# Kernel optimization log

Hardware: AMD Instinct MI355X
Metric: run time of the kernel (lower is better)

The kernel has to match this reference:

```python
import jax, jax.numpy as jnp
import numpy as np

B, S, E, H = 4, 512, 512, 8
DH = E // H
HID = max(16, E // 4)  # sr_ratio=4
ALPHA = 0.1
EPS_SAFE = 0.05  # eps=1e-6 clamped to [0.05, 0.8]


def _xavier(k, shape):
    fan_out, fan_in = shape[0], shape[1]
    lim = (6.0 / (fan_in + fan_out)) ** 0.5
    return jax.random.uniform(k, shape, minval=-lim, maxval=lim, dtype=jnp.float32)


def setup_inputs() -> dict:
    key = jax.random.key(0)
    ks = jax.random.split(key, 8)
    return {
        "x": jax.random.normal(ks[0], (B, S, E), dtype=jnp.float32),
        "wq": _xavier(ks[1], (E, E)), "bq": jnp.zeros((E,), jnp.float32),
        "wk": _xavier(ks[2], (E, E)), "bk": jnp.zeros((E,), jnp.float32),
        "wv": _xavier(ks[3], (E, E)), "bv": jnp.zeros((E,), jnp.float32),
        "wo": _xavier(ks[4], (E, E)), "bo": jnp.zeros((E,), jnp.float32),
        # sr_conv1: Conv2d(1, HID, 1) -> weight [HID,1,1,1] == vector [HID]
        "w1": _xavier(ks[5], (HID, 1)).reshape(HID), "b1": jnp.zeros((HID,), jnp.float32),
        # sr_conv2: Conv2d(HID, 1, 1) -> weight [1,HID,1,1] == vector [HID]
        "w2": _xavier(ks[6], (1, HID)).reshape(HID), "b2": jnp.zeros((), jnp.float32),
    }


def _autopoietic_transform(scores, w1, b1, w2, b2):
    # scores: [B, H, S, S]
    scores = jnp.clip(jnp.nan_to_num(scores, nan=0.0, posinf=10.0, neginf=-10.0), -15.0, 15.0)
    mean_attn = scores.mean(axis=1)  # mean over heads -> [B, S, S]

    scaled = jnp.clip(jnp.clip(mean_attn, -8.0, 8.0) * EPS_SAFE, -10.0, 10.0)
    # conv1x1 (1 -> HID): broadcastmul; clamp + relu; conv1x1 (HID -> 1)
    hid = scaled[:, None, :, :] * w1[None, :, None, None] + b1[None, :, None, None]  # [B,HID,S,S]
    hid = jax.nn.relu(jnp.clip(hid, -5.0, 5.0))
    auto = jnp.einsum('bhij,h->bij', hid, w2) + b2  # [B,S,S]
    auto = jnp.clip(auto, -5.0, 5.0)

    # Taylor expansion with clamp, then sigmoid smoothing
    taylor = jnp.clip(1.0 + 0.05 * (auto * 50.0), 0.5, 1.5)
    sig = jax.nn.sigmoid(taylor)

    # fuzzy probability via entropy of softmax of mean attention
    p = jax.nn.softmax(jnp.clip(mean_attn, -10.0, 10.0), axis=-1)
    Hent = -p * jnp.log(p + 1e-6)
    Fm = jax.nn.softmax(3.0 * Hent, axis=-1)

    t = sig * Fm

    # energy (Frobenius-norm) balancing per batch
    e_o = jnp.sqrt((mean_attn ** 2).sum(axis=(1, 2))) + 1e-4
    e_t = jnp.sqrt((t ** 2).sum(axis=(1, 2))) + 1e-4
    gamma = jnp.clip(e_o / e_t, 0.8, 1.2)[:, None, None]
    t = gamma * t

    # dynamic std matching
    t_mean = t.mean(axis=(1, 2), keepdims=True)
    o_mean = mean_attn.mean(axis=(1, 2), keepdims=True)
    t_std = jnp.sqrt(jnp.clip(((t - t_mean) ** 2).mean(axis=(1, 2), keepdims=True), 0.01, None))
    o_std = jnp.sqrt(jnp.clip(((mean_attn - o_mean) ** 2).mean(axis=(1, 2), keepdims=True), 0.01, None))
    gdyn = jnp.clip(o_std / t_std, 0.8, 1.2)
    t = o_mean + gdyn * (t - t_mean)

    # residual blend of transformed map back into per-head scores (alpha=0.1), final clamp
    return jnp.clip(scores + ALPHA * t[:, None, :, :], -15.0, 15.0)


def reference(x, wq, bq, wk, bk, wv, bv, wo, bo, w1, b1, w2, b2):
    scaling = DH ** -0.5
    q = (jnp.einsum('bse,oe->bso', x, wq) + bq).reshape(B, S, H, DH).transpose(0, 2, 1, 3) * scaling
    k = (jnp.einsum('bse,oe->bso', x, wk) + bk).reshape(B, S, H, DH).transpose(0, 2, 1, 3)
    v = (jnp.einsum('bse,oe->bso', x, wv) + bv).reshape(B, S, H, DH).transpose(0, 2, 1, 3)
    scores = jnp.einsum('bhqd,bhkd->bhqk', q, k)  # [B,H,S,S]
    scores = _autopoietic_transform(scores, w1, b1, w2, b2)
    attn = jax.nn.softmax(scores, axis=-1)
    out = jnp.einsum('bhqk,bhkd->bhqd', attn, v).transpose(0, 2, 1, 3).reshape(B, S, E)
    return jnp.einsum('bse,oe->bso', out, wo) + bo
```

## Files before the change

kernel.cpp:

```cpp
#include <hip/hip_runtime.h>
#include <math.h>

#define BATCH 4
#define SEQ   512
#define EMB   512
#define NH    8
#define DHD   64
#define HIDN  128
#define ALPHA 0.1f
#define EPSS  0.05f

#define LUTN  2048
#define XMIN  (-0.4f)
#define XSTEP (0.8f / LUTN)

typedef __attribute__((ext_vector_type(8))) short  bf16x8;
typedef __attribute__((ext_vector_type(4))) float  f32x4;
#define MFMA(a,b,c) __builtin_amdgcn_mfma_f32_16x16x32_bf16((a),(b),(c),0,0,0)

__device__ __forceinline__ unsigned short f2bf(float f) {
    union { float f; unsigned u; } v; v.f = f;
    unsigned r = v.u + 0x7fffu + ((v.u >> 16) & 1u);
    return (unsigned short)(r >> 16);
}
__device__ __forceinline__ float bf2f(unsigned short h) {
    union { unsigned u; float f; } v; v.u = ((unsigned)h) << 16;
    return v.f;
}
__device__ __forceinline__ float f16tof(unsigned short h) {
    union { unsigned short s; _Float16 f; } v; v.s = h; return (float)v.f;
}
__device__ __forceinline__ unsigned short ftof16(float f) {
    union { unsigned short s; _Float16 f; } v; v.f = (_Float16)f; return v.s;
}

__device__ __forceinline__ void async_lds16(const unsigned short* g, unsigned short* l) {
    __builtin_amdgcn_global_load_lds(
        (const __attribute__((address_space(1))) void*)g,
        (__attribute__((address_space(3))) void*)l, 16, 0, 0);
}

template<int KS, int UN, int MT>
__device__ __forceinline__ void gemm_core64(
    const unsigned short* __restrict__ A, const unsigned short* __restrict__ B,
    int m0, int n0, unsigned short* sA, unsigned short* sB, f32x4 (&acc)[2][4])
{
    const int K = KS * 64;
    const int tid = threadIdx.x, w = tid >> 6, lane = tid & 63;
    const int quad = lane >> 4, r = lane & 15;
    const int wm = w >> 1, wn = w & 1;
    const int lrow = lane >> 3, lc = lane & 7;
    const int sc = lc ^ lrow;
    constexpr int AF = MT / 32;
    constexpr int NB = UN;

    const unsigned short* ag[2]; unsigned short* dAu[2];
    #pragma unroll
    for (int c = 0; c < AF; c++) {
        const int rb = w * (8 * AF) + c * 8;
        ag[c]  = A + (long)(m0 + rb + lrow) * K + sc * 8;
        dAu[c] = sA + rb * 64;
    }
    const unsigned short* bg[4]; unsigned short* dBu[4];
    #pragma unroll
    for (int c = 0; c < NB; c++) {
        const int rb = w * (8 * NB) + c * 8;
        bg[c]  = B + (long)(n0 + rb + lrow) * K + sc * 8;
        dBu[c] = sB + rb * 64;
    }

    for (int s = 0; s < KS; s++) {
        const int k0 = s * 64;
        #pragma unroll
        for (int c = 0; c < AF; c++) async_lds16(ag[c] + k0, dAu[c]);
        #pragma unroll
        for (int c = 0; c < NB; c++) async_lds16(bg[c] + k0, dBu[c]);
        __syncthreads();
        #pragma unroll
        for (int kc = 0; kc < 2; kc++) {
            bf16x8 af[2], bfr[4];
            #pragma unroll
            for (int t = 0; t < AF; t++) {
                const int row = wm * (16 * AF) + t * 16 + r;
                af[t] = *(const bf16x8*)(sA + row * 64 + ((kc * 4 + quad) ^ (row & 7)) * 8);
            }
            #pragma unroll
            for (int u = 0; u < UN; u++) {
                const int row = wn * (16 * UN) + u * 16 + r;
                bfr[u] = *(const bf16x8*)(sB + row * 64 + ((kc * 4 + quad) ^ (row & 7)) * 8);
            }
            #pragma unroll
            for (int t = 0; t < AF; t++)
                #pragma unroll
                for (int u = 0; u < UN; u++)
                    acc[t][u] = MFMA(af[t], bfr[u], acc[t][u]);
        }
        __syncthreads();
    }
}

__global__ __launch_bounds__(256) void gemm_qkv(
    const unsigned short* __restrict__ x_ext, const unsigned short* __restrict__ w_ext,
    const float* __restrict__ bq, const float* __restrict__ bk, const float* __restrict__ bv,
    unsigned short* __restrict__ q_ext, unsigned short* __restrict__ k_ext,
    unsigned short* __restrict__ vT)
{
    __shared__ __align__(16) unsigned char smem[64 * 68 * 4];
    unsigned short* sA = (unsigned short*)smem;
    unsigned short* sB = (unsigned short*)(smem + 64 * 64 * 2);
    float* sC = (float*)smem;

    const int m0 = blockIdx.y * 64, n0 = blockIdx.x * 64;
    f32x4 acc[2][4] = {};
    gemm_core64<24, 2, 64>(x_ext, w_ext, m0, n0, sA, sB, acc);

    const int tid = threadIdx.x, w = tid >> 6, lane = tid & 63;
    const int quad = lane >> 4, r = lane & 15;
    const int wm = w >> 1, wn = w & 1;
    #pragma unroll
    for (int t = 0; t < 2; t++)
        #pragma unroll
        for (int u = 0; u < 2; u++)
            #pragma unroll
            for (int g = 0; g < 4; g++)
                sC[(wm * 32 + t * 16 + quad * 4 + g) * 68 + wn * 32 + u * 16 + r] = acc[t][u][g];
    __syncthreads();

    const int which = n0 >> 9;
    const int n0l = n0 & 511;
    const int h0 = n0l >> 6;
    const int b = m0 >> 9, s0 = m0 & 511;

    if (which < 2) {
        const float scl = (which == 0) ? 0.125f : 1.0f;
        const float* bias = (which == 0) ? bq : bk;
        unsigned* dst = (unsigned*)((which == 0) ? q_ext : k_ext);
        #pragma unroll
        for (int seg = 0; seg < 3; seg++) {
            const bool lo = (which == 0) ? (seg == 1) : (seg == 2);
            #pragma unroll
            for (int it = 0; it < 8; it++) {
                const int idx = it * 256 + tid;
                const int sl = idx >> 5;
                const int jc = idx & 31;
                const int nc = jc * 2;
                float v0 = (sC[sl * 68 + nc]     + bias[n0l + nc])     * scl;
                float v1 = (sC[sl * 68 + nc + 1] + bias[n0l + nc + 1]) * scl;
                unsigned short a0 = f2bf(v0), a1 = f2bf(v1);
                if (lo) { a0 = f2bf(v0 - bf2f(a0)); a1 = f2bf(v1 - bf2f(a1)); }
                const long orow = (long)(b * NH + h0) * SEQ + s0 + sl;
                dst[orow * 96 + seg * 32 + jc] = (unsigned)a0 | ((unsigned)a1 << 16);
            }
        }
    } else {
        unsigned* dst = (unsigned*)vT;
        #pragma unroll
        for (int it = 0; it < 8; it++) {
            const int idx = it * 256 + tid;
            const int d = idx >> 5;
            const int jc = idx & 31;
            const int sl = jc * 2;
            const float bvv = bv[n0l + d];
            const float v0 = sC[sl * 68 + d] + bvv;
            const float v1 = sC[(sl + 1) * 68 + d] + bvv;
            const long orow = (long)(b * NH + h0) * DHD + d;
            dst[orow * 256 + (s0 >> 1) + jc] = (unsigned)f2bf(v0) | ((unsigned)f2bf(v1) << 16);
        }
    }
}

__global__ __launch_bounds__(256) void gemm_scores(
    const unsigned short* __restrict__ q_ext, const unsigned short* __restrict__ k_ext,
    unsigned short* __restrict__ scoresH)
{
    __shared__ __align__(16) unsigned short sA[64 * 64];
    __shared__ __align__(16) unsigned short sB[128 * 64];
    const int z = blockIdx.z;
    const int m0 = blockIdx.y * 64, n0 = blockIdx.x * 128;
    f32x4 acc[2][4] = {};
    gemm_core64<3, 4, 64>(q_ext + (long)z * SEQ * 192, k_ext + (long)z * SEQ * 192,
                          m0, n0, sA, sB, acc);

    const int tid = threadIdx.x, w = tid >> 6, lane = tid & 63;
    const int quad = lane >> 4, r = lane & 15;
    const int wm = w >> 1, wn = w & 1;
    unsigned short* hC = sB;
    #pragma unroll
    for (int t = 0; t < 2; t++)
        #pragma unroll
        for (int u = 0; u < 4; u++)
            #pragma unroll
            for (int g = 0; g < 4; g++) {
                const int ml = wm * 32 + t * 16 + quad * 4 + g;
                const int nl = wn * 64 + u * 16 + r;
                hC[ml * 128 + nl] = ftof16(fminf(fmaxf(acc[t][u][g], -15.f), 15.f));
            }
    __syncthreads();
    #pragma unroll
    for (int it = 0; it < 4; it++) {
        const int id = it * 256 + tid;
        const int ml = id >> 4, ch = id & 15;
        *(uint4*)(scoresH + ((long)z * SEQ + m0 + ml) * SEQ + n0 + ch * 8) =
            *(const uint4*)(hC + ml * 128 + ch * 8);
    }
}

__global__ __launch_bounds__(256) void gemm_proj(
    const unsigned short* __restrict__ otmp, const unsigned short* __restrict__ woh,
    const float* __restrict__ bo, float* __restrict__ out)
{
    __shared__ __align__(16) unsigned short sA[32 * 64];
    __shared__ __align__(16) unsigned short sB[64 * 64];
    const int m0 = blockIdx.y * 32, n0 = blockIdx.x * 64;
    f32x4 acc[2][4] = {};
    gemm_core64<8, 2, 32>(otmp, woh, m0, n0, sA, sB, acc);
    const int tid = threadIdx.x, w = tid >> 6, lane = tid & 63;
    const int quad = lane >> 4, r = lane & 15;
    const int wm = w >> 1, wn = w & 1;
    #pragma unroll
    for (int u = 0; u < 2; u++)
        #pragma unroll
        for (int g = 0; g < 4; g++) {
            const int m = m0 + wm * 16 + quad * 4 + g;
            const int n = n0 + wn * 32 + u * 16 + r;
            out[(long)m * EMB + n] = acc[0][u][g] + bo[n];
        }
}

__device__ __forceinline__ float blockReduceSum(float v, float* sred) {
    #pragma unroll
    for (int o = 32; o > 0; o >>= 1) v += __shfl_down(v, o);
    __syncthreads();
    if ((threadIdx.x & 63) == 0) sred[threadIdx.x >> 6] = v;
    __syncthreads();
    return (sred[0] + sred[1]) + (sred[2] + sred[3]);
}
__device__ __forceinline__ float4 blockReduceSum4(float4 v, float4* s4) {
    #pragma unroll
    for (int o = 32; o > 0; o >>= 1) {
        v.x += __shfl_down(v.x, o); v.y += __shfl_down(v.y, o);
        v.z += __shfl_down(v.z, o); v.w += __shfl_down(v.w, o);
    }
    __syncthreads();
    if ((threadIdx.x & 63) == 0) s4[threadIdx.x >> 6] = v;
    __syncthreads();
    float4 r;
    r.x = (s4[0].x + s4[1].x) + (s4[2].x + s4[3].x);
    r.y = (s4[0].y + s4[1].y) + (s4[2].y + s4[3].y);
    r.z = (s4[0].z + s4[1].z) + (s4[2].z + s4[3].z);
    r.w = (s4[0].w + s4[1].w) + (s4[2].w + s4[3].w);
    return r;
}

__global__ __launch_bounds__(256) void prep_kernel(
    const float* __restrict__ x,
    const float* __restrict__ wq, const float* __restrict__ wk,
    const float* __restrict__ wv, const float* __restrict__ wo,
    const float* __restrict__ w1, const float* __restrict__ b1,
    const float* __restrict__ w2, const float* __restrict__ b2,
    unsigned short* __restrict__ x_ext, unsigned short* __restrict__ w_ext,
    unsigned short* __restrict__ woh, float* __restrict__ lut)
{
    const int blk = blockIdx.x;
    if (blk < 9) {
        const int i = blk * 256 + threadIdx.x;
        if (i > LUTN) return;
        const float xv = XMIN + i * XSTEP;
        float a = 0.f;
        for (int h = 0; h < HIDN; h++) {
            float hv = xv * w1[h] + b1[h];
            hv = fminf(fmaxf(hv, -5.f), 5.f);
            hv = fmaxf(hv, 0.f);
            a += hv * w2[h];
        }
        a += b2[0];
        a = fminf(fmaxf(a, -5.f), 5.f);
        const float taylor = fminf(fmaxf(1.f + 2.5f * a, 0.5f), 1.5f);
        lut[i] = 1.f / (1.f + expf(-taylor));
        return;
    }
    const int i = (blk - 9) * 256 + threadIdx.x;
    if (i < 262144) {
        const int m = i >> 7, kq = i & 127;
        const float4 v = ((const float4*)x)[i];
        const unsigned short h0 = f2bf(v.x), h1 = f2bf(v.y), h2 = f2bf(v.z), h3 = f2bf(v.w);
        const unsigned hi01 = (unsigned)h0 | ((unsigned)h1 << 16);
        const unsigned hi23 = (unsigned)h2 | ((unsigned)h3 << 16);
        const unsigned lo01 = (unsigned)f2bf(v.x - bf2f(h0)) | ((unsigned)f2bf(v.y - bf2f(h1)) << 16);
        const unsigned lo23 = (unsigned)f2bf(v.z - bf2f(h2)) | ((unsigned)f2bf(v.w - bf2f(h3)) << 16);
        unsigned* dst = (unsigned*)x_ext;
        const long base = (long)m * 768 + kq * 2;
        dst[base] = hi01;       dst[base + 1] = hi23;
        dst[base + 256] = lo01; dst[base + 257] = lo23;
        dst[base + 512] = hi01; dst[base + 513] = hi23;
    } else if (i < 458752) {
        const int j = i - 262144;
        const int n = j >> 7, kq = j & 127;
        const float4 v = (j < 65536) ? ((const float4*)wq)[j]
                       : (j < 131072 ? ((const float4*)wk)[j - 65536]
                                     : ((const float4*)wv)[j - 131072]);
        const unsigned short h0 = f2bf(v.x), h1 = f2bf(v.y), h2 = f2bf(v.z), h3 = f2bf(v.w);
        const unsigned hi01 = (unsigned)h0 | ((unsigned)h1 << 16);
        const unsigned hi23 = (unsigned)h2 | ((unsigned)h3 << 16);
        const unsigned lo01 = (unsigned)f2bf(v.x - bf2f(h0)) | ((unsigned)f2bf(v.y - bf2f(h1)) << 16);
        const unsigned lo23 = (unsigned)f2bf(v.z - bf2f(h2)) | ((unsigned)f2bf(v.w - bf2f(h3)) << 16);
        unsigned* dst = (unsigned*)w_ext;
        const long base = (long)n * 768 + kq * 2;
        dst[base] = hi01;       dst[base + 1] = hi23;
        dst[base + 256] = hi01; dst[base + 257] = hi23;
        dst[base + 512] = lo01; dst[base + 513] = lo23;
    } else {
        const int j = i - 458752;
        const float4 v = ((const float4*)wo)[j];
        unsigned* dst = (unsigned*)woh;
        dst[j * 2]     = (unsigned)f2bf(v.x) | ((unsigned)f2bf(v.y) << 16);
        dst[j * 2 + 1] = (unsigned)f2bf(v.z) | ((unsigned)f2bf(v.w) << 16);
    }
}

__global__ __launch_bounds__(256) void transform_kernel(
    const unsigned short* __restrict__ scoresH,
    const float* __restrict__ lut,
    unsigned short* __restrict__ t0H,
    float4* __restrict__ partials)
{
    const int rr = blockIdx.x;
    const int b = rr >> 9, i = rr & 511;
    const int tid = threadIdx.x;

    __shared__ float slut[LUTN + 1];
    __shared__ float sred[4];
    __shared__ float4 sred4[4];

    for (int u = tid; u <= LUTN; u += 256) slut[u] = lut[u];

    const unsigned* baseU =
        (const unsigned*)(scoresH + (((long)(b * NH)) * SEQ + i) * SEQ) + tid;
    float s0 = 0.f, s1 = 0.f;
    #pragma unroll
    for (int h = 0; h < NH; h++) {
        const unsigned pv = baseU[h * (SEQ * SEQ / 2)];
        s0 += f16tof((unsigned short)pv);
        s1 += f16tof((unsigned short)(pv >> 16));
    }
    float mv[2] = { s0 * 0.125f, s1 * 0.125f };
    __syncthreads();

    float sigv[2], ex[2];
    float lsum = 0.f;
    #pragma unroll
    for (int u = 0; u < 2; u++) {
        const float m = mv[u];
        const float x = fminf(fmaxf(m, -8.f), 8.f) * EPSS;
        float t = (x - XMIN) * (1.0f / XSTEP);
        int idx = (int)t;
        idx = idx < 0 ? 0 : (idx > LUTN - 1 ? LUTN - 1 : idx);
        const float frac = t - (float)idx;
        const float l0 = slut[idx], l1 = slut[idx + 1];
        sigv[u] = l0 + frac * (l1 - l0);
        ex[u] = expf(fminf(fmaxf(m, -10.f), 10.f));
        lsum += ex[u];
    }
    const float rsum = blockReduceSum(lsum, sred);
    const float inv = 1.f / rsum;

    float ex2[2], lsum2 = 0.f;
    #pragma unroll
    for (int u = 0; u < 2; u++) {
        const float p = ex[u] * inv;
        const float he = -p * logf(p + 1e-6f);
        ex2[u] = expf(3.f * he);
        lsum2 += ex2[u];
    }
    const float rsum2 = blockReduceSum(lsum2, sred);
    const float inv2 = 1.f / rsum2;

    float tv[2];
    #pragma unroll
    for (int u = 0; u < 2; u++) tv[u] = sigv[u] * (ex2[u] * inv2);
    ((unsigned*)t0H)[((long)b * SEQ + i) * (SEQ / 2) + tid] =
        (unsigned)ftof16(tv[0]) | ((unsigned)ftof16(tv[1]) << 16);

    float4 pv;
    pv.x = mv[0] + mv[1];
    pv.y = mv[0] * mv[0] + mv[1] * mv[1];
    pv.z = tv[0] + tv[1];
    pv.w = tv[0] * tv[0] + tv[1] * tv[1];
    const float4 rs = blockReduceSum4(pv, sred4);
    if (tid == 0) partials[rr] = rs;
}

__global__ __launch_bounds__(256) void softmax_attnv(
    const unsigned short* __restrict__ scoresH,
    const unsigned short* __restrict__ t0H,
    const float4* __restrict__ partials,
    const unsigned short* __restrict__ vT,
    unsigned short* __restrict__ otmp)
{
    __shared__ __align__(16) unsigned char smem[40960];
    unsigned short* attnS = (unsigned short*)smem;
    unsigned short* sB    = (unsigned short*)(smem + 32768);
    float*  sC    = (float*)smem;
    float4* sred4 = (float4*)smem;

    const int m0 = blockIdx.x * 32;
    const int z  = blockIdx.y;
    const int b  = z >> 3, h = z & 7;
    const int tid = threadIdx.x, wv = tid >> 6, lane = tid & 63;

    const float4 p0 = partials[b * SEQ + tid];
    const float4 p1 = partials[b * SEQ + tid + 256];
    float4 pv4 = make_float4(p0.x + p1.x, p0.y + p1.y, p0.z + p1.z, p0.w + p1.w);
    const float4 rs4 = blockReduceSum4(pv4, sred4);
    const float sm = rs4.x, sm2 = rs4.y, st = rs4.z, st2 = rs4.w;
    const float n = (float)SEQ * (float)SEQ;
    const float gamma = fminf(fmaxf((sqrtf(sm2) + 1e-4f) / (sqrtf(st2) + 1e-4f), 0.8f), 1.2f);
    const float o_mean = sm / n, t0m = st / n;
    const float o_std = sqrtf(fmaxf(fmaxf(sm2 / n - o_mean * o_mean, 0.f), 0.01f));
    const float t_std = sqrtf(fmaxf(gamma * gamma * fmaxf(st2 / n - t0m * t0m, 0.f), 0.01f));
    const float gdyn = fminf(fmaxf(o_std / t_std, 0.8f), 1.2f);
    const float c1 = gdyn * gamma;
    const float c0 = o_mean - c1 * t0m;
    __syncthreads();

    const int lrow = lane >> 3, lc = lane & 7;
    const int scw = lc ^ lrow;
    const unsigned short* bg0 = vT + (long)z * DHD * SEQ + (long)(wv * 16 + lrow) * SEQ + scw * 8;
    const unsigned short* bg1 = bg0 + 8 * SEQ;
    unsigned short* dB0 = sB + (wv * 16) * 64;
    unsigned short* dB1 = sB + (wv * 16 + 8) * 64;
    async_lds16(bg0, dB0);
    async_lds16(bg1, dB1);

    const int j0 = lane * 8;
    for (int it = 0; it < 8; it++) {
        const int rowl = it * 4 + wv;
        const bf16x8 sr = *(const bf16x8*)(scoresH + ((long)z * SEQ + m0 + rowl) * SEQ + j0);
        const bf16x8 tr = *(const bf16x8*)(t0H + ((long)b * SEQ + m0 + rowl) * SEQ + j0);
        float sv[8];
        float lsum = 0.f;
        #pragma unroll
        for (int u = 0; u < 8; u++) {
            float s = f16tof((unsigned short)sr[u])
                    + ALPHA * (c0 + c1 * f16tof((unsigned short)tr[u]));
            s = fminf(fmaxf(s, -15.f), 15.f);
            sv[u] = expf(s);
            lsum += sv[u];
        }
        #pragma unroll
        for (int o = 32; o > 0; o >>= 1) lsum += __shfl_down(lsum, o);
        lsum = __shfl(lsum, 0);
        const float inv = 1.f / lsum;
        bf16x8 pk;
        #pragma unroll
        for (int u = 0; u < 8; u++) pk[u] = (short)f2bf(sv[u] * inv);
        *(bf16x8*)(attnS + rowl * 512 + (j0 ^ ((rowl & 7) << 3))) = pk;
    }

    const int quad = lane >> 4, r = lane & 15;
    const int wm = wv >> 1, wn = wv & 1;
    const int arow = wm * 16 + r;
    const int aswz = (arow & 7) << 3;
    f32x4 acc[2] = {};
    for (int s = 0; s < 8; s++) {
        __syncthreads();
        const int k0 = s * 64;
        #pragma unroll
        for (int kc = 0; kc < 2; kc++) {
            const bf16x8 a = *(const bf16x8*)(attnS + arow * 512 + ((k0 + kc * 32 + quad * 8) ^ aswz));
            #pragma unroll
            for (int u = 0; u < 2; u++) {
                const int row = wn * 32 + u * 16 + r;
                const bf16x8 bb = *(const bf16x8*)(sB + row * 64 + ((kc * 4 + quad) ^ (row & 7)) * 8);
                acc[u] = MFMA(a, bb, acc[u]);
            }
        }
        __syncthreads();
        if (s < 7) { async_lds16(bg0 + (s + 1) * 64, dB0); async_lds16(bg1 + (s + 1) * 64, dB1); }
    }

    #pragma unroll
    for (int u = 0; u < 2; u++)
        #pragma unroll
        for (int g = 0; g < 4; g++)
            sC[(wm * 16 + quad * 4 + g) * 66 + wn * 32 + u * 16 + r] = acc[u][g];
    __syncthreads();
    unsigned* dst = (unsigned*)otmp;
    #pragma unroll
    for (int it = 0; it < 4; it++) {
        const int idx = it * 256 + tid;
        const int sr2 = idx >> 5, jc = idx & 31;
        const float v0 = sC[sr2 * 66 + jc * 2], v1 = sC[sr2 * 66 + jc * 2 + 1];
        dst[((long)(b * SEQ + m0 + sr2)) * 256 + h * 32 + jc] =
            (unsigned)f2bf(v0) | ((unsigned)f2bf(v1) << 16);
    }
}

extern "C" void kernel_launch(void* const* d_in, const int* in_sizes, int n_in,
                              void* d_out, int out_size, void* d_ws, size_t ws_size,
                              hipStream_t stream) {
    const float* x  = (const float*)d_in[0];
    const float* wq = (const float*)d_in[1];
    const float* bq = (const float*)d_in[2];
    const float* wk = (const float*)d_in[3];
    const float* bk = (const float*)d_in[4];
    const float* wv = (const float*)d_in[5];
    const float* bv = (const float*)d_in[6];
    const float* wo = (const float*)d_in[7];
    const float* bo = (const float*)d_in[8];
    const float* w1 = (const float*)d_in[9];
    const float* b1 = (const float*)d_in[10];
    const float* w2 = (const float*)d_in[11];
    const float* b2 = (const float*)d_in[12];
    float* out = (float*)d_out;

    char* wsb = (char*)d_ws;
    unsigned short* scoresH = (unsigned short*)wsb;
    unsigned short* t0H     = scoresH + 8388608;
    float4* partials = (float4*)(t0H + 1048576);
    float*  lutbuf   = (float*)(partials + 2048);
    unsigned short* u16 = (unsigned short*)(wsb + (20u << 20));
    unsigned short* x_ext = u16;
    unsigned short* w_ext = x_ext + 3145728;
    unsigned short* q_ext = w_ext + 2359296;
    unsigned short* k_ext = q_ext + 3145728;
    unsigned short* vT    = k_ext + 3145728;
    unsigned short* otmp  = vT + 1048576;
    unsigned short* woh   = otmp + 1048576;

    prep_kernel<<<dim3(9 + 2048), dim3(256), 0, stream>>>(
        x, wq, wk, wv, wo, w1, b1, w2, b2, x_ext, w_ext, woh, lutbuf);

    gemm_qkv<<<dim3(24, 32), dim3(256), 0, stream>>>(
        x_ext, w_ext, bq, bk, bv, q_ext, k_ext, vT);

    gemm_scores<<<dim3(4, 8, 32), dim3(256), 0, stream>>>(q_ext, k_ext, scoresH);

    transform_kernel<<<dim3(BATCH * SEQ), dim3(256), 0, stream>>>(
        scoresH, lutbuf, t0H, partials);

    softmax_attnv<<<dim3(16, 32), dim3(256), 0, stream>>>(
        scoresH, t0H, partials, vT, otmp);

    gemm_proj<<<dim3(8, 64), dim3(256), 0, stream>>>(otmp, woh, bo, out);
}
```

Before: 145.5 us.

## Fuse output projection into attention kernel via per-head atomic accumulation

The separate output-projection GEMM is removed. Each attention block now multiplies its 32x64 per-head output tile by the matching 64-column slice of Wo and atomically adds the result into the zero-initialised output, with the bias added only by head 0. The transform kernel is also changed to handle four rows per block so the LUT is loaded into shared memory fewer times. This drops one launch and the otmp round-trip through memory, but adds a memset, eight-way float atomic contention per output element, uncached Wo reads straight from global memory, and nondeterministic summation order.

```diff
diff --git a/kernel.cpp b/kernel.cpp
--- a/kernel.cpp
+++ b/kernel.cpp
@@ -203,28 +203,6 @@
         *(uint4*)(scoresH + ((long)z * SEQ + m0 + ml) * SEQ + n0 + ch * 8) =
             *(const uint4*)(hC + ml * 128 + ch * 8);
     }
-}
-
-__global__ __launch_bounds__(256) void gemm_proj(
-    const unsigned short* __restrict__ otmp, const unsigned short* __restrict__ woh,
-    const float* __restrict__ bo, float* __restrict__ out)
-{
-    __shared__ __align__(16) unsigned short sA[32 * 64];
-    __shared__ __align__(16) unsigned short sB[64 * 64];
-    const int m0 = blockIdx.y * 32, n0 = blockIdx.x * 64;
-    f32x4 acc[2][4] = {};
-    gemm_core64<8, 2, 32>(otmp, woh, m0, n0, sA, sB, acc);
-    const int tid = threadIdx.x, w = tid >> 6, lane = tid & 63;
-    const int quad = lane >> 4, r = lane & 15;
-    const int wm = w >> 1, wn = w & 1;
-    #pragma unroll
-    for (int u = 0; u < 2; u++)
-        #pragma unroll
-        for (int g = 0; g < 4; g++) {
-            const int m = m0 + wm * 16 + quad * 4 + g;
-            const int n = n0 + wn * 32 + u * 16 + r;
-            out[(long)m * EMB + n] = acc[0][u][g] + bo[n];
-        }
 }
 
 __device__ __forceinline__ float blockReduceSum(float v, float* sred) {
@@ -324,8 +302,6 @@
     unsigned short* __restrict__ t0H,
     float4* __restrict__ partials)
 {
-    const int rr = blockIdx.x;
-    const int b = rr >> 9, i = rr & 511;
     const int tid = threadIdx.x;
 
     __shared__ float slut[LUTN + 1];
@@ -333,74 +309,81 @@
     __shared__ float4 sred4[4];
 
     for (int u = tid; u <= LUTN; u += 256) slut[u] = lut[u];
-
-    const unsigned* baseU =
-        (const unsigned*)(scoresH + (((long)(b * NH)) * SEQ + i) * SEQ) + tid;
-    float s0 = 0.f, s1 = 0.f;
-    #pragma unroll
-    for (int h = 0; h < NH; h++) {
-        const unsigned pv = baseU[h * (SEQ * SEQ / 2)];
-        s0 += f16tof((unsigned short)pv);
-        s1 += f16tof((unsigned short)(pv >> 16));
-    }
-    float mv[2] = { s0 * 0.125f, s1 * 0.125f };
-    __syncthreads();
-
-    float sigv[2], ex[2];
-    float lsum = 0.f;
-    #pragma unroll
-    for (int u = 0; u < 2; u++) {
-        const float m = mv[u];
-        const float x = fminf(fmaxf(m, -8.f), 8.f) * EPSS;
-        float t = (x - XMIN) * (1.0f / XSTEP);
-        int idx = (int)t;
-        idx = idx < 0 ? 0 : (idx > LUTN - 1 ? LUTN - 1 : idx);
-        const float frac = t - (float)idx;
-        const float l0 = slut[idx], l1 = slut[idx + 1];
-        sigv[u] = l0 + frac * (l1 - l0);
-        ex[u] = expf(fminf(fmaxf(m, -10.f), 10.f));
-        lsum += ex[u];
-    }
-    const float rsum = blockReduceSum(lsum, sred);
-    const float inv = 1.f / rsum;
-
-    float ex2[2], lsum2 = 0.f;
-    #pragma unroll
-    for (int u = 0; u < 2; u++) {
-        const float p = ex[u] * inv;
-        const float he = -p * logf(p + 1e-6f);
-        ex2[u] = expf(3.f * he);
-        lsum2 += ex2[u];
-    }
-    const float rsum2 = blockReduceSum(lsum2, sred);
-    const float inv2 = 1.f / rsum2;
-
-    float tv[2];
-    #pragma unroll
-    for (int u = 0; u < 2; u++) tv[u] = sigv[u] * (ex2[u] * inv2);
-    ((unsigned*)t0H)[((long)b * SEQ + i) * (SEQ / 2) + tid] =
-        (unsigned)ftof16(tv[0]) | ((unsigned)ftof16(tv[1]) << 16);
-
-    float4 pv;
-    pv.x = mv[0] + mv[1];
-    pv.y = mv[0] * mv[0] + mv[1] * mv[1];
-    pv.z = tv[0] + tv[1];
-    pv.w = tv[0] * tv[0] + tv[1] * tv[1];
-    const float4 rs = blockReduceSum4(pv, sred4);
-    if (tid == 0) partials[rr] = rs;
-}
-
-__global__ __launch_bounds__(256) void softmax_attnv(
+    __syncthreads();
+
+    for (int r4 = 0; r4 < 4; r4++) {
+        const int rr = blockIdx.x * 4 + r4;
+        const int b = rr >> 9, i = rr & 511;
+
+        const unsigned* baseU =
+            (const unsigned*)(scoresH + (((long)(b * NH)) * SEQ + i) * SEQ) + tid;
+        float s0 = 0.f, s1 = 0.f;
+        #pragma unroll
+        for (int h = 0; h < NH; h++) {
+            const unsigned pv = baseU[h * (SEQ * SEQ / 2)];
+            s0 += f16tof((unsigned short)pv);
+            s1 += f16tof((unsigned short)(pv >> 16));
+        }
+        float mv[2] = { s0 * 0.125f, s1 * 0.125f };
+
+        float sigv[2], ex[2];
+        float lsum = 0.f;
+        #pragma unroll
+        for (int u = 0; u < 2; u++) {
+            const float m = mv[u];
+            const float x = fminf(fmaxf(m, -8.f), 8.f) * EPSS;
+            float t = (x - XMIN) * (1.0f / XSTEP);
+            int idx = (int)t;
+            idx = idx < 0 ? 0 : (idx > LUTN - 1 ? LUTN - 1 : idx);
+            const float frac = t - (float)idx;
+            const float l0 = slut[idx], l1 = slut[idx + 1];
+            sigv[u] = l0 + frac * (l1 - l0);
+            ex[u] = expf(fminf(fmaxf(m, -10.f), 10.f));
+            lsum += ex[u];
+        }
+        const float rsum = blockReduceSum(lsum, sred);
+        const float inv = 1.f / rsum;
+
+        float ex2[2], lsum2 = 0.f;
+        #pragma unroll
+        for (int u = 0; u < 2; u++) {
+            const float p = ex[u] * inv;
+            const float he = -p * logf(p + 1e-6f);
+            ex2[u] = expf(3.f * he);
+            lsum2 += ex2[u];
+        }
+        const float rsum2 = blockReduceSum(lsum2, sred);
+        const float inv2 = 1.f / rsum2;
+
+        float tv[2];
+        #pragma unroll
+        for (int u = 0; u < 2; u++) tv[u] = sigv[u] * (ex2[u] * inv2);
+        ((unsigned*)t0H)[((long)b * SEQ + i) * (SEQ / 2) + tid] =
+            (unsigned)ftof16(tv[0]) | ((unsigned)ftof16(tv[1]) << 16);
+
+        float4 pv;
+        pv.x = mv[0] + mv[1];
+        pv.y = mv[0] * mv[0] + mv[1] * mv[1];
+        pv.z = tv[0] + tv[1];
+        pv.w = tv[0] * tv[0] + tv[1] * tv[1];
+        const float4 rs = blockReduceSum4(pv, sred4);
+        if (tid == 0) partials[rr] = rs;
+    }
+}
+
+__global__ __launch_bounds__(256) void softmax_attnv_proj(
     const unsigned short* __restrict__ scoresH,
     const unsigned short* __restrict__ t0H,
     const float4* __restrict__ partials,
     const unsigned short* __restrict__ vT,
-    unsigned short* __restrict__ otmp)
+    const unsigned short* __restrict__ woh,
+    const float* __restrict__ bo,
+    float* __restrict__ out)
 {
     __shared__ __align__(16) unsigned char smem[40960];
     unsigned short* attnS = (unsigned short*)smem;
     unsigned short* sB    = (unsigned short*)(smem + 32768);
-    float*  sC    = (float*)smem;
+    unsigned short* oA    = (unsigned short*)smem;
     float4* sred4 = (float4*)smem;
 
     const int m0 = blockIdx.x * 32;
@@ -483,16 +466,31 @@
     for (int u = 0; u < 2; u++)
         #pragma unroll
         for (int g = 0; g < 4; g++)
-            sC[(wm * 16 + quad * 4 + g) * 66 + wn * 32 + u * 16 + r] = acc[u][g];
-    __syncthreads();
-    unsigned* dst = (unsigned*)otmp;
-    #pragma unroll
-    for (int it = 0; it < 4; it++) {
-        const int idx = it * 256 + tid;
-        const int sr2 = idx >> 5, jc = idx & 31;
-        const float v0 = sC[sr2 * 66 + jc * 2], v1 = sC[sr2 * 66 + jc * 2 + 1];
-        dst[((long)(b * SEQ + m0 + sr2)) * 256 + h * 32 + jc] =
-            (unsigned)f2bf(v0) | ((unsigned)f2bf(v1) << 16);
+            oA[(wm * 16 + quad * 4 + g) * 72 + wn * 32 + u * 16 + r] = f2bf(acc[u][g]);
+    __syncthreads();
+
+    for (int nc = 0; nc < 8; nc++) {
+        f32x4 acc2[2] = {};
+        #pragma unroll
+        for (int kc = 0; kc < 2; kc++) {
+            const bf16x8 a = *(const bf16x8*)(oA + (wm * 16 + r) * 72 + kc * 32 + quad * 8);
+            #pragma unroll
+            for (int u = 0; u < 2; u++) {
+                const int nrow = nc * 64 + wn * 32 + u * 16 + r;
+                const bf16x8 bb = *(const bf16x8*)(woh + (long)nrow * EMB + h * 64 + kc * 32 + quad * 8);
+                acc2[u] = MFMA(a, bb, acc2[u]);
+            }
+        }
+        #pragma unroll
+        for (int u = 0; u < 2; u++)
+            #pragma unroll
+            for (int g = 0; g < 4; g++) {
+                const int m = m0 + wm * 16 + quad * 4 + g;
+                const int nn = nc * 64 + wn * 32 + u * 16 + r;
+                float v = acc2[u][g];
+                if (h == 0) v += bo[nn];
+                atomicAdd(out + (long)(b * SEQ + m) * EMB + nn, v);
+            }
     }
 }
 
@@ -525,8 +523,9 @@
     unsigned short* q_ext = w_ext + 2359296;
     unsigned short* k_ext = q_ext + 3145728;
     unsigned short* vT    = k_ext + 3145728;
-    unsigned short* otmp  = vT + 1048576;
-    unsigned short* woh   = otmp + 1048576;
+    unsigned short* woh   = vT + 1048576;
+
+    hipMemsetAsync(out, 0, (size_t)BATCH * SEQ * EMB * sizeof(float), stream);
 
     prep_kernel<<<dim3(9 + 2048), dim3(256), 0, stream>>>(
         x, wq, wk, wv, wo, w1, b1, w2, b2, x_ext, w_ext, woh, lutbuf);
@@ -536,11 +535,9 @@
 
     gemm_scores<<<dim3(4, 8, 32), dim3(256), 0, stream>>>(q_ext, k_ext, scoresH);
 
-    transform_kernel<<<dim3(BATCH * SEQ), dim3(256), 0, stream>>>(
+    transform_kernel<<<dim3(512), dim3(256), 0, stream>>>(
         scoresH, lutbuf, t0H, partials);
 
-    softmax_attnv<<<dim3(16, 32), dim3(256), 0, stream>>>(
-        scoresH, t0H, partials, vT, otmp);
-
-    gemm_proj<<<dim3(8, 64), dim3(256), 0, stream>>>(otmp, woh, bo, out);
-}
+    softmax_attnv_proj<<<dim3(16, 32), dim3(256), 0, stream>>>(
+        scoresH, t0H, partials, vT, woh, bo, out);
+}
```

Measured after the change: 175.1 us. +20.4%, slower.

## Load GEMM B operands directly from global and batch transform rows per block

Applied to the files above, without the earlier changes.

The output projection and the attn·V stage now read MFMA B fragments (and, for the projection, A fragments) straight from global memory. This replaces LDS staging with async copies and barriers. The transform kernel processes four rows per block and launches a quarter as many blocks, so the 8 KB LUT load into shared memory is amortized. The trade is uncoalesced, L2-dependent global fragment loads in place of shared-memory reuse, and less parallelism in the transform stage.

```diff
diff --git a/kernel.cpp b/kernel.cpp
--- a/kernel.cpp
+++ b/kernel.cpp
@@ -209,21 +209,32 @@
     const unsigned short* __restrict__ otmp, const unsigned short* __restrict__ woh,
     const float* __restrict__ bo, float* __restrict__ out)
 {
-    __shared__ __align__(16) unsigned short sA[32 * 64];
-    __shared__ __align__(16) unsigned short sB[64 * 64];
     const int m0 = blockIdx.y * 32, n0 = blockIdx.x * 64;
-    f32x4 acc[2][4] = {};
-    gemm_core64<8, 2, 32>(otmp, woh, m0, n0, sA, sB, acc);
     const int tid = threadIdx.x, w = tid >> 6, lane = tid & 63;
     const int quad = lane >> 4, r = lane & 15;
     const int wm = w >> 1, wn = w & 1;
+
+    const unsigned short* aB = otmp + (long)(m0 + wm * 16 + r) * EMB + quad * 8;
+    const unsigned short* bB0 = woh + (long)(n0 + wn * 32 + r) * EMB + quad * 8;
+    const unsigned short* bB1 = bB0 + 16 * EMB;
+
+    f32x4 acc[2] = {};
+    #pragma unroll 4
+    for (int kc = 0; kc < 16; kc++) {
+        const int k = kc * 32;
+        const bf16x8 a  = *(const bf16x8*)(aB + k);
+        const bf16x8 b0 = *(const bf16x8*)(bB0 + k);
+        const bf16x8 b1 = *(const bf16x8*)(bB1 + k);
+        acc[0] = MFMA(a, b0, acc[0]);
+        acc[1] = MFMA(a, b1, acc[1]);
+    }
     #pragma unroll
     for (int u = 0; u < 2; u++)
         #pragma unroll
         for (int g = 0; g < 4; g++) {
             const int m = m0 + wm * 16 + quad * 4 + g;
             const int n = n0 + wn * 32 + u * 16 + r;
-            out[(long)m * EMB + n] = acc[0][u][g] + bo[n];
+            out[(long)m * EMB + n] = acc[u][g] + bo[n];
         }
 }
 
@@ -324,8 +335,6 @@
     unsigned short* __restrict__ t0H,
     float4* __restrict__ partials)
 {
-    const int rr = blockIdx.x;
-    const int b = rr >> 9, i = rr & 511;
     const int tid = threadIdx.x;
 
     __shared__ float slut[LUTN + 1];
@@ -333,61 +342,66 @@
     __shared__ float4 sred4[4];
 
     for (int u = tid; u <= LUTN; u += 256) slut[u] = lut[u];
-
-    const unsigned* baseU =
-        (const unsigned*)(scoresH + (((long)(b * NH)) * SEQ + i) * SEQ) + tid;
-    float s0 = 0.f, s1 = 0.f;
-    #pragma unroll
-    for (int h = 0; h < NH; h++) {
-        const unsigned pv = baseU[h * (SEQ * SEQ / 2)];
-        s0 += f16tof((unsigned short)pv);
-        s1 += f16tof((unsigned short)(pv >> 16));
-    }
-    float mv[2] = { s0 * 0.125f, s1 * 0.125f };
-    __syncthreads();
-
-    float sigv[2], ex[2];
-    float lsum = 0.f;
-    #pragma unroll
-    for (int u = 0; u < 2; u++) {
-        const float m = mv[u];
-        const float x = fminf(fmaxf(m, -8.f), 8.f) * EPSS;
-        float t = (x - XMIN) * (1.0f / XSTEP);
-        int idx = (int)t;
-        idx = idx < 0 ? 0 : (idx > LUTN - 1 ? LUTN - 1 : idx);
-        const float frac = t - (float)idx;
-        const float l0 = slut[idx], l1 = slut[idx + 1];
-        sigv[u] = l0 + frac * (l1 - l0);
-        ex[u] = expf(fminf(fmaxf(m, -10.f), 10.f));
-        lsum += ex[u];
-    }
-    const float rsum = blockReduceSum(lsum, sred);
-    const float inv = 1.f / rsum;
-
-    float ex2[2], lsum2 = 0.f;
-    #pragma unroll
-    for (int u = 0; u < 2; u++) {
-        const float p = ex[u] * inv;
-        const float he = -p * logf(p + 1e-6f);
-        ex2[u] = expf(3.f * he);
-        lsum2 += ex2[u];
-    }
-    const float rsum2 = blockReduceSum(lsum2, sred);
-    const float inv2 = 1.f / rsum2;
-
-    float tv[2];
-    #pragma unroll
-    for (int u = 0; u < 2; u++) tv[u] = sigv[u] * (ex2[u] * inv2);
-    ((unsigned*)t0H)[((long)b * SEQ + i) * (SEQ / 2) + tid] =
-        (unsigned)ftof16(tv[0]) | ((unsigned)ftof16(tv[1]) << 16);
-
-    float4 pv;
-    pv.x = mv[0] + mv[1];
-    pv.y = mv[0] * mv[0] + mv[1] * mv[1];
-    pv.z = tv[0] + tv[1];
-    pv.w = tv[0] * tv[0] + tv[1] * tv[1];
-    const float4 rs = blockReduceSum4(pv, sred4);
-    if (tid == 0) partials[rr] = rs;
+    __syncthreads();
+
+    for (int r4 = 0; r4 < 4; r4++) {
+        const int rr = blockIdx.x * 4 + r4;
+        const int b = rr >> 9, i = rr & 511;
+
+        const unsigned* baseU =
+            (const unsigned*)(scoresH + (((long)(b * NH)) * SEQ + i) * SEQ) + tid;
+        float s0 = 0.f, s1 = 0.f;
+        #pragma unroll
+        for (int h = 0; h < NH; h++) {
+            const unsigned pv = baseU[h * (SEQ * SEQ / 2)];
+            s0 += f16tof((unsigned short)pv);
+            s1 += f16tof((unsigned short)(pv >> 16));
+        }
+        float mv[2] = { s0 * 0.125f, s1 * 0.125f };
+
+        float sigv[2], ex[2];
+        float lsum = 0.f;
+        #pragma unroll
+        for (int u = 0; u < 2; u++) {
+            const float m = mv[u];
+            const float x = fminf(fmaxf(m, -8.f), 8.f) * EPSS;
+            float t = (x - XMIN) * (1.0f / XSTEP);
+            int idx = (int)t;
+            idx = idx < 0 ? 0 : (idx > LUTN - 1 ? LUTN - 1 : idx);
+            const float frac = t - (float)idx;
+            const float l0 = slut[idx], l1 = slut[idx + 1];
+            sigv[u] = l0 + frac * (l1 - l0);
+            ex[u] = expf(fminf(fmaxf(m, -10.f), 10.f));
+            lsum += ex[u];
+        }
+        const float rsum = blockReduceSum(lsum, sred);
+        const float inv = 1.f / rsum;
+
+        float ex2[2], lsum2 = 0.f;
+        #pragma unroll
+        for (int u = 0; u < 2; u++) {
+            const float p = ex[u] * inv;
+            const float he = -p * logf(p + 1e-6f);
+            ex2[u] = expf(3.f * he);
+            lsum2 += ex2[u];
+        }
+        const float rsum2 = blockReduceSum(lsum2, sred);
+        const float inv2 = 1.f / rsum2;
+
+        float tv[2];
+        #pragma unroll
+        for (int u = 0; u < 2; u++) tv[u] = sigv[u] * (ex2[u] * inv2);
+        ((unsigned*)t0H)[((long)b * SEQ + i) * (SEQ / 2) + tid] =
+            (unsigned)ftof16(tv[0]) | ((unsigned)ftof16(tv[1]) << 16);
+
+        float4 pv;
+        pv.x = mv[0] + mv[1];
+        pv.y = mv[0] * mv[0] + mv[1] * mv[1];
+        pv.z = tv[0] + tv[1];
+        pv.w = tv[0] * tv[0] + tv[1] * tv[1];
+        const float4 rs = blockReduceSum4(pv, sred4);
+        if (tid == 0) partials[rr] = rs;
+    }
 }
 
 __global__ __launch_bounds__(256) void softmax_attnv(
@@ -397,9 +411,8 @@
     const unsigned short* __restrict__ vT,
     unsigned short* __restrict__ otmp)
 {
-    __shared__ __align__(16) unsigned char smem[40960];
+    __shared__ __align__(16) unsigned char smem[32768];
     unsigned short* attnS = (unsigned short*)smem;
-    unsigned short* sB    = (unsigned short*)(smem + 32768);
     float*  sC    = (float*)smem;
     float4* sred4 = (float4*)smem;
 
@@ -423,15 +436,6 @@
     const float c0 = o_mean - c1 * t0m;
     __syncthreads();
 
-    const int lrow = lane >> 3, lc = lane & 7;
-    const int scw = lc ^ lrow;
-    const unsigned short* bg0 = vT + (long)z * DHD * SEQ + (long)(wv * 16 + lrow) * SEQ + scw * 8;
-    const unsigned short* bg1 = bg0 + 8 * SEQ;
-    unsigned short* dB0 = sB + (wv * 16) * 64;
-    unsigned short* dB1 = sB + (wv * 16 + 8) * 64;
-    async_lds16(bg0, dB0);
-    async_lds16(bg1, dB1);
-
     const int j0 = lane * 8;
     for (int it = 0; it < 8; it++) {
         const int rowl = it * 4 + wv;
@@ -456,28 +460,29 @@
         for (int u = 0; u < 8; u++) pk[u] = (short)f2bf(sv[u] * inv);
         *(bf16x8*)(attnS + rowl * 512 + (j0 ^ ((rowl & 7) << 3))) = pk;
     }
+    __syncthreads();
 
     const int quad = lane >> 4, r = lane & 15;
     const int wm = wv >> 1, wn = wv & 1;
     const int arow = wm * 16 + r;
     const int aswz = (arow & 7) << 3;
+    const unsigned short* vB0 = vT + (long)z * DHD * SEQ + (long)(wn * 32 + r) * SEQ + quad * 8;
+    const unsigned short* vB1 = vB0 + 16 * SEQ;
     f32x4 acc[2] = {};
+    #pragma unroll 2
     for (int s = 0; s < 8; s++) {
-        __syncthreads();
         const int k0 = s * 64;
         #pragma unroll
         for (int kc = 0; kc < 2; kc++) {
-            const bf16x8 a = *(const bf16x8*)(attnS + arow * 512 + ((k0 + kc * 32 + quad * 8) ^ aswz));
-            #pragma unroll
-            for (int u = 0; u < 2; u++) {
-                const int row = wn * 32 + u * 16 + r;
-                const bf16x8 bb = *(const bf16x8*)(sB + row * 64 + ((kc * 4 + quad) ^ (row & 7)) * 8);
-                acc[u] = MFMA(a, bb, acc[u]);
-            }
-        }
-        __syncthreads();
-        if (s < 7) { async_lds16(bg0 + (s + 1) * 64, dB0); async_lds16(bg1 + (s + 1) * 64, dB1); }
-    }
+            const int k = k0 + kc * 32;
+            const bf16x8 a  = *(const bf16x8*)(attnS + arow * 512 + ((k + quad * 8) ^ aswz));
+            const bf16x8 b0 = *(const bf16x8*)(vB0 + k);
+            const bf16x8 b1 = *(const bf16x8*)(vB1 + k);
+            acc[0] = MFMA(a, b0, acc[0]);
+            acc[1] = MFMA(a, b1, acc[1]);
+        }
+    }
+    __syncthreads();
 
     #pragma unroll
     for (int u = 0; u < 2; u++)
@@ -536,7 +541,7 @@
 
     gemm_scores<<<dim3(4, 8, 32), dim3(256), 0, stream>>>(q_ext, k_ext, scoresH);
 
-    transform_kernel<<<dim3(BATCH * SEQ), dim3(256), 0, stream>>>(
+    transform_kernel<<<dim3(512), dim3(256), 0, stream>>>(
         scoresH, lutbuf, t0H, partials);
 
     softmax_attnv<<<dim3(16, 32), dim3(256), 0, stream>>>(
```

Measured after the change: 158.2 us. 1.09x slower.

## Fuse bf16 split-precision conversion into GEMMs and drop prep kernel

Applied to the files above, without the earlier changes.

Removes the separate prep kernel. The fp32-to-bf16 hi/lo splitting of x and the QKV weights now happens inside gemm_qkv while tiles are staged into LDS, and the wo conversion happens inside gemm_proj, which now reads operands straight from global memory without LDS. The LUT construction moves into a few gemm_scores blocks. This saves one launch and the round trip of the extended buffers through memory, at the cost of synchronous fp32 loads in place of async LDS loads and of redoing the conversion for every tile.

```diff
diff --git a/kernel.cpp b/kernel.cpp
--- a/kernel.cpp
+++ b/kernel.cpp
@@ -38,6 +38,17 @@
     __builtin_amdgcn_global_load_lds(
         (const __attribute__((address_space(1))) void*)g,
         (__attribute__((address_space(3))) void*)l, 16, 0, 0);
+}
+
+__device__ __forceinline__ bf16x8 pack8(const float4 v0, const float4 v1, bool lo) {
+    const float vv[8] = { v0.x, v0.y, v0.z, v0.w, v1.x, v1.y, v1.z, v1.w };
+    bf16x8 pk;
+    #pragma unroll
+    for (int i = 0; i < 8; i++) {
+        const unsigned short h = f2bf(vv[i]);
+        pk[i] = (short)(lo ? f2bf(vv[i] - bf2f(h)) : h);
+    }
+    return pk;
 }
 
 template<int KS, int UN, int MT>
@@ -100,7 +111,8 @@
 }
 
 __global__ __launch_bounds__(256) void gemm_qkv(
-    const unsigned short* __restrict__ x_ext, const unsigned short* __restrict__ w_ext,
+    const float* __restrict__ x,
+    const float* __restrict__ wq, const float* __restrict__ wk, const float* __restrict__ wv,
     const float* __restrict__ bq, const float* __restrict__ bk, const float* __restrict__ bv,
     unsigned short* __restrict__ q_ext, unsigned short* __restrict__ k_ext,
     unsigned short* __restrict__ vT)
@@ -111,12 +123,61 @@
     float* sC = (float*)smem;
 
     const int m0 = blockIdx.y * 64, n0 = blockIdx.x * 64;
-    f32x4 acc[2][4] = {};
-    gemm_core64<24, 2, 64>(x_ext, w_ext, m0, n0, sA, sB, acc);
-
     const int tid = threadIdx.x, w = tid >> 6, lane = tid & 63;
     const int quad = lane >> 4, r = lane & 15;
     const int wm = w >> 1, wn = w & 1;
+    const int lrow = lane >> 3, lc = lane & 7;
+    const int sc = lc ^ lrow;
+
+    const int which = n0 >> 9;
+    const int n0l = n0 & 511;
+    const float* wbase = (which == 0) ? wq : (which == 1) ? wk : wv;
+
+    f32x4 acc[2][4] = {};
+    for (int s = 0; s < 24; s++) {
+        const int seg = s >> 3;
+        const int kk = (s & 7) * 64 + sc * 8;
+        const bool loA = (seg == 1);
+        const bool loB = (seg == 2);
+        #pragma unroll
+        for (int c = 0; c < 2; c++) {
+            const int rb = w * 16 + c * 8;
+            const float* src = x + (long)(m0 + rb + lrow) * 512 + kk;
+            const float4 v0 = *(const float4*)src;
+            const float4 v1 = *(const float4*)(src + 4);
+            *(bf16x8*)(sA + (rb + lrow) * 64 + lc * 8) = pack8(v0, v1, loA);
+        }
+        #pragma unroll
+        for (int c = 0; c < 2; c++) {
+            const int rb = w * 16 + c * 8;
+            const float* src = wbase + (long)(n0l + rb + lrow) * 512 + kk;
+            const float4 v0 = *(const float4*)src;
+            const float4 v1 = *(const float4*)(src + 4);
+            *(bf16x8*)(sB + (rb + lrow) * 64 + lc * 8) = pack8(v0, v1, loB);
+        }
+        __syncthreads();
+        #pragma unroll
+        for (int kc = 0; kc < 2; kc++) {
+            bf16x8 af[2], bfr[2];
+            #pragma unroll
+            for (int t = 0; t < 2; t++) {
+                const int row = wm * 32 + t * 16 + r;
+                af[t] = *(const bf16x8*)(sA + row * 64 + ((kc * 4 + quad) ^ (row & 7)) * 8);
+            }
+            #pragma unroll
+            for (int u = 0; u < 2; u++) {
+                const int row = wn * 32 + u * 16 + r;
+                bfr[u] = *(const bf16x8*)(sB + row * 64 + ((kc * 4 + quad) ^ (row & 7)) * 8);
+            }
+            #pragma unroll
+            for (int t = 0; t < 2; t++)
+                #pragma unroll
+                for (int u = 0; u < 2; u++)
+                    acc[t][u] = MFMA(af[t], bfr[u], acc[t][u]);
+        }
+        __syncthreads();
+    }
+
     #pragma unroll
     for (int t = 0; t < 2; t++)
         #pragma unroll
@@ -126,8 +187,6 @@
                 sC[(wm * 32 + t * 16 + quad * 4 + g) * 68 + wn * 32 + u * 16 + r] = acc[t][u][g];
     __syncthreads();
 
-    const int which = n0 >> 9;
-    const int n0l = n0 & 511;
     const int h0 = n0l >> 6;
     const int b = m0 >> 9, s0 = m0 & 511;
 
@@ -171,12 +230,34 @@
 
 __global__ __launch_bounds__(256) void gemm_scores(
     const unsigned short* __restrict__ q_ext, const unsigned short* __restrict__ k_ext,
+    const float* __restrict__ w1, const float* __restrict__ b1,
+    const float* __restrict__ w2, const float* __restrict__ b2,
+    float* __restrict__ lut,
     unsigned short* __restrict__ scoresH)
 {
     __shared__ __align__(16) unsigned short sA[64 * 64];
     __shared__ __align__(16) unsigned short sB[128 * 64];
     const int z = blockIdx.z;
     const int m0 = blockIdx.y * 64, n0 = blockIdx.x * 128;
+
+    if (blockIdx.x == 0 && blockIdx.y == 0 && z < 9) {
+        const int i = z * 256 + threadIdx.x;
+        if (i <= LUTN) {
+            const float xv = XMIN + i * XSTEP;
+            float a = 0.f;
+            for (int h = 0; h < HIDN; h++) {
+                float hv = xv * w1[h] + b1[h];
+                hv = fminf(fmaxf(hv, -5.f), 5.f);
+                hv = fmaxf(hv, 0.f);
+                a += hv * w2[h];
+            }
+            a += b2[0];
+            a = fminf(fmaxf(a, -5.f), 5.f);
+            const float taylor = fminf(fmaxf(1.f + 2.5f * a, 0.5f), 1.5f);
+            lut[i] = 1.f / (1.f + expf(-taylor));
+        }
+    }
+
     f32x4 acc[2][4] = {};
     gemm_core64<3, 4, 64>(q_ext + (long)z * SEQ * 192, k_ext + (long)z * SEQ * 192,
                           m0, n0, sA, sB, acc);
@@ -206,24 +287,35 @@
 }
 
 __global__ __launch_bounds__(256) void gemm_proj(
-    const unsigned short* __restrict__ otmp, const unsigned short* __restrict__ woh,
+    const unsigned short* __restrict__ otmp, const float* __restrict__ wo,
     const float* __restrict__ bo, float* __restrict__ out)
 {
-    __shared__ __align__(16) unsigned short sA[32 * 64];
-    __shared__ __align__(16) unsigned short sB[64 * 64];
     const int m0 = blockIdx.y * 32, n0 = blockIdx.x * 64;
-    f32x4 acc[2][4] = {};
-    gemm_core64<8, 2, 32>(otmp, woh, m0, n0, sA, sB, acc);
     const int tid = threadIdx.x, w = tid >> 6, lane = tid & 63;
     const int quad = lane >> 4, r = lane & 15;
     const int wm = w >> 1, wn = w & 1;
+
+    const unsigned short* aB = otmp + (long)(m0 + wm * 16 + r) * EMB + quad * 8;
+    const float* wB0 = wo + (long)(n0 + wn * 32 + r) * EMB + quad * 8;
+    const float* wB1 = wB0 + 16 * EMB;
+
+    f32x4 acc[2] = {};
+    #pragma unroll 4
+    for (int kc = 0; kc < 16; kc++) {
+        const int k = kc * 32;
+        const bf16x8 a = *(const bf16x8*)(aB + k);
+        const bf16x8 b0 = pack8(*(const float4*)(wB0 + k), *(const float4*)(wB0 + k + 4), false);
+        const bf16x8 b1 = pack8(*(const float4*)(wB1 + k), *(const float4*)(wB1 + k + 4), false);
+        acc[0] = MFMA(a, b0, acc[0]);
+        acc[1] = MFMA(a, b1, acc[1]);
+    }
     #pragma unroll
     for (int u = 0; u < 2; u++)
         #pragma unroll
         for (int g = 0; g < 4; g++) {
             const int m = m0 + wm * 16 + quad * 4 + g;
             const int n = n0 + wn * 32 + u * 16 + r;
-            out[(long)m * EMB + n] = acc[0][u][g] + bo[n];
+            out[(long)m * EMB + n] = acc[u][g] + bo[n];
         }
 }
 
@@ -250,72 +342,6 @@
     r.z = (s4[0].z + s4[1].z) + (s4[2].z + s4[3].z);
     r.w = (s4[0].w + s4[1].w) + (s4[2].w + s4[3].w);
     return r;
-}
-
-__global__ __launch_bounds__(256) void prep_kernel(
-    const float* __restrict__ x,
-    const float* __restrict__ wq, const float* __restrict__ wk,
-    const float* __restrict__ wv, const float* __restrict__ wo,
-    const float* __restrict__ w1, const float* __restrict__ b1,
-    const float* __restrict__ w2, const float* __restrict__ b2,
-    unsigned short* __restrict__ x_ext, unsigned short* __restrict__ w_ext,
-    unsigned short* __restrict__ woh, float* __restrict__ lut)
-{
-    const int blk = blockIdx.x;
-    if (blk < 9) {
-        const int i = blk * 256 + threadIdx.x;
-        if (i > LUTN) return;
-        const float xv = XMIN + i * XSTEP;
-        float a = 0.f;
-        for (int h = 0; h < HIDN; h++) {
-            float hv = xv * w1[h] + b1[h];
-            hv = fminf(fmaxf(hv, -5.f), 5.f);
-            hv = fmaxf(hv, 0.f);
-            a += hv * w2[h];
-        }
-        a += b2[0];
-        a = fminf(fmaxf(a, -5.f), 5.f);
-        const float taylor = fminf(fmaxf(1.f + 2.5f * a, 0.5f), 1.5f);
-        lut[i] = 1.f / (1.f + expf(-taylor));
-        return;
-    }
-    const int i = (blk - 9) * 256 + threadIdx.x;
-    if (i < 262144) {
-        const int m = i >> 7, kq = i & 127;
-        const float4 v = ((const float4*)x)[i];
-        const unsigned short h0 = f2bf(v.x), h1 = f2bf(v.y), h2 = f2bf(v.z), h3 = f2bf(v.w);
-        const unsigned hi01 = (unsigned)h0 | ((unsigned)h1 << 16);
-        const unsigned hi23 = (unsigned)h2 | ((unsigned)h3 << 16);
-        const unsigned lo01 = (unsigned)f2bf(v.x - bf2f(h0)) | ((unsigned)f2bf(v.y - bf2f(h1)) << 16);
-        const unsigned lo23 = (unsigned)f2bf(v.z - bf2f(h2)) | ((unsigned)f2bf(v.w - bf2f(h3)) << 16);
-        unsigned* dst = (unsigned*)x_ext;
-        const long base = (long)m * 768 + kq * 2;
-        dst[base] = hi01;       dst[base + 1] = hi23;
-        dst[base + 256] = lo01; dst[base + 257] = lo23;
-        dst[base + 512] = hi01; dst[base + 513] = hi23;
-    } else if (i < 458752) {
-        const int j = i - 262144;
-        const int n = j >> 7, kq = j & 127;
-        const float4 v = (j < 65536) ? ((const float4*)wq)[j]
-                       : (j < 131072 ? ((const float4*)wk)[j - 65536]
-                                     : ((const float4*)wv)[j - 131072]);
-        const unsigned short h0 = f2bf(v.x), h1 = f2bf(v.y), h2 = f2bf(v.z), h3 = f2bf(v.w);
-        const unsigned hi01 = (unsigned)h0 | ((unsigned)h1 << 16);
-        const unsigned hi23 = (unsigned)h2 | ((unsigned)h3 << 16);
-        const unsigned lo01 = (unsigned)f2bf(v.x - bf2f(h0)) | ((unsigned)f2bf(v.y - bf2f(h1)) << 16);
-        const unsigned lo23 = (unsigned)f2bf(v.z - bf2f(h2)) | ((unsigned)f2bf(v.w - bf2f(h3)) << 16);
-        unsigned* dst = (unsigned*)w_ext;
-        const long base = (long)n * 768 + kq * 2;
-        dst[base] = hi01;       dst[base + 1] = hi23;
-        dst[base + 256] = hi01; dst[base + 257] = hi23;
-        dst[base + 512] = lo01; dst[base + 513] = lo23;
-    } else {
-        const int j = i - 458752;
-        const float4 v = ((const float4*)wo)[j];
-        unsigned* dst = (unsigned*)woh;
-        dst[j * 2]     = (unsigned)f2bf(v.x) | ((unsigned)f2bf(v.y) << 16);
-        dst[j * 2 + 1] = (unsigned)f2bf(v.z) | ((unsigned)f2bf(v.w) << 16);
-    }
 }
 
 __global__ __launch_bounds__(256) void transform_kernel(
@@ -520,21 +546,16 @@
     float4* partials = (float4*)(t0H + 1048576);
     float*  lutbuf   = (float*)(partials + 2048);
     unsigned short* u16 = (unsigned short*)(wsb + (20u << 20));
-    unsigned short* x_ext = u16;
-    unsigned short* w_ext = x_ext + 3145728;
-    unsigned short* q_ext = w_ext + 2359296;
+    unsigned short* q_ext = u16;
     unsigned short* k_ext = q_ext + 3145728;
     unsigned short* vT    = k_ext + 3145728;
     unsigned short* otmp  = vT + 1048576;
-    unsigned short* woh   = otmp + 1048576;
-
-    prep_kernel<<<dim3(9 + 2048), dim3(256), 0, stream>>>(
-        x, wq, wk, wv, wo, w1, b1, w2, b2, x_ext, w_ext, woh, lutbuf);
 
     gemm_qkv<<<dim3(24, 32), dim3(256), 0, stream>>>(
-        x_ext, w_ext, bq, bk, bv, q_ext, k_ext, vT);
-
-    gemm_scores<<<dim3(4, 8, 32), dim3(256), 0, stream>>>(q_ext, k_ext, scoresH);
+        x, wq, wk, wv, bq, bk, bv, q_ext, k_ext, vT);
+
+    gemm_scores<<<dim3(4, 8, 32), dim3(256), 0, stream>>>(
+        q_ext, k_ext, w1, b1, w2, b2, lutbuf, scoresH);
 
     transform_kernel<<<dim3(BATCH * SEQ), dim3(256), 0, stream>>>(
         scoresH, lutbuf, t0H, partials);
@@ -542,5 +563,5 @@
     softmax_attnv<<<dim3(16, 32), dim3(256), 0, stream>>>(
         scoresH, t0H, partials, vT, otmp);
 
-    gemm_proj<<<dim3(8, 64), dim3(256), 0, stream>>>(otmp, woh, bo, out);
-}
+    gemm_proj<<<dim3(8, 64), dim3(256), 0, stream>>>(otmp, wo, bo, out);
+}
```

Result: slower. 184.3 us (+26.7%).
